# Optimization experiments

Measured on AMD Instinct MI355X. Metric: run time of the kernel, lower is better.

## Reference

```python
import jax, jax.numpy as jnp
import numpy as np

EPS = 1e-5

def gcn_conv(x, W, b, src, dst, ew, N):
    # PyG GCNConv: linear, add self-loops (weight 1), symmetric norm, aggregate, + bias
    xw = x @ W                                            # [N, C]
    deg = jax.ops.segment_sum(ew, dst, num_segments=N) + 1.0
    dis = jax.lax.rsqrt(deg)                              # deg^{-1/2}, deg >= 1
    coef = dis[src] * dis[dst] * ew                       # [E]
    msg = jax.ops.segment_sum(coef[:, None] * xw[src], dst, num_segments=N)
    return msg + (dis * dis)[:, None] * xw + b            # self-loop term + bias


def stride_pool(x, src, dst, ew, stride):
    # pad nodes to multiple of stride with zeros, mean over groups of `stride`,
    # keep only edges whose endpoints are both multiples of stride (weight mask)
    N, C = x.shape
    newN = -(-N // stride)
    pad = newN * stride - N
    if pad > 0:
        x = jnp.concatenate([x, jnp.zeros((pad, C), x.dtype)], axis=0)
    x = x.reshape(newN, stride, C).mean(axis=1)
    mask = (src % stride == 0) & (dst % stride == 0)
    src = jnp.minimum(src // stride, newN - 1)
    dst = jnp.minimum(dst // stride, newN - 1)
    ew = ew * mask.astype(ew.dtype)
    return x, src, dst, ew, newN


def bn_relu(x, g, b):
    # BatchNorm1d in training mode: batch stats over node dim, biased variance
    mu = x.mean(axis=0)
    var = x.var(axis=0)
    return jax.nn.relu((x - mu) * jax.lax.rsqrt(var + EPS) * g + b)


def setup_inputs() -> dict:
    key = jax.random.key(0)
    ks = jax.random.split(key, 16)
    N, E = 100000, 1600000
    inp = {
        'x': jax.random.normal(ks[0], (N, 1), jnp.float32),
        'W1': jax.random.normal(ks[1], (1, 64), jnp.float32) * 0.5,
        'b1': jax.random.normal(ks[2], (64,), jnp.float32) * 0.1,
        'g1': jnp.ones((64,), jnp.float32), 'be1': jnp.zeros((64,), jnp.float32),
        'W2': jax.random.normal(ks[3], (64, 64), jnp.float32) * 0.125,
        'b2': jax.random.normal(ks[4], (64,), jnp.float32) * 0.1,
        'g2': jnp.ones((64,), jnp.float32), 'be2': jnp.zeros((64,), jnp.float32),
        'W3': jax.random.normal(ks[5], (64, 64), jnp.float32) * 0.125,
        'b3': jax.random.normal(ks[6], (64,), jnp.float32) * 0.1,
        'g3': jnp.ones((64,), jnp.float32), 'be3': jnp.zeros((64,), jnp.float32),
        'W4': jax.random.normal(ks[7], (64, 64), jnp.float32) * 0.125,
        'b4': jax.random.normal(ks[8], (64,), jnp.float32) * 0.1,
        'g4': jnp.ones((64,), jnp.float32), 'be4': jnp.zeros((64,), jnp.float32),
        'fcW1': jax.random.normal(ks[9], (64, 128), jnp.float32) * 0.125,
        'fcb1': jax.random.normal(ks[10], (128,), jnp.float32) * 0.1,
        'fcW2': jax.random.normal(ks[11], (128, 10), jnp.float32) * 0.09,
        'fcb2': jax.random.normal(ks[12], (10,), jnp.float32) * 0.1,
        'src': jax.random.randint(ks[13], (E,), 0, N, jnp.int32).astype(jnp.int64),
        'dst': jax.random.randint(ks[14], (E,), 0, N, jnp.int32).astype(jnp.int64),
        'batch': jnp.zeros((N,), jnp.int64),
    }
    return inp


def reference(x, W1, b1, g1, be1, W2, b2, g2, be2, W3, b3, g3, be3,
              W4, b4, g4, be4, fcW1, fcb1, fcW2, fcb2, src, dst, batch):
    N0 = x.shape[0]
    ew = jnp.ones(src.shape, x.dtype)
    N = N0
    strides = [2, 2, 3, 3]
    params = [(W1, b1, g1, be1), (W2, b2, g2, be2), (W3, b3, g3, be3), (W4, b4, g4, be4)]
    for (W, b, g, be), s in zip(params, strides):
        x = gcn_conv(x, W, b, src, dst, ew, N)
        x, src, dst, ew, N = stride_pool(x, src, dst, ew, s)
        x = bn_relu(x, g, be)
    # pad back to original node count with zeros
    pad = N0 - x.shape[0]
    if pad > 0:
        x = jnp.concatenate([x, jnp.zeros((pad, x.shape[1]), x.dtype)], axis=0)
    # batch remapped to arange(N0) => global_mean_pool is identity
    x = jax.nn.relu(x @ fcW1 + fcb1)
    return x @ fcW2 + fcb2   # [N0, 10]
```

## Files before the change

kernel.cpp:

```cpp
#include <hip/hip_runtime.h>
#include <hip/hip_bf16.h>

#define GEPS 1e-5f

#define NN0 100000
#define NN1 50000
#define NN2 25000
#define NN3 8334
#define NN4 2778
#define BASE2 0
#define BASE3 50000
#define BASE4 75000
#define CNT_TOT 83334
#define CAPTOT 688128
#define NB 391
#define CAP_B 5120
#define BIN_CH 4096

__device__ __forceinline__ void atomAddF(float* p, float v) {
  unsafeAtomicAdd(p, v);
}

__device__ __forceinline__ unsigned ld_idx(const int* a, int e, int f64) {
  return (unsigned)(f64 ? a[2 * e] : a[e]);
}

__device__ __forceinline__ unsigned f2bf(float f) {
  unsigned b = __float_as_uint(f);
  return (b + 0x8000u) >> 16;
}

__global__ void gcn_init(int* cntAll, float* sumbuf, int* gcur, int* flag, const int* src) {
  int i = blockIdx.x * 256 + threadIdx.x;
  if (i == 0) {
    int o = src[1] | src[3] | src[5] | src[7] | src[9] | src[11] | src[13] | src[15];
    flag[0] = (o == 0) ? 1 : 0;
  }
  if (i < CNT_TOT) cntAll[i] = 0;
  if (i < 512) sumbuf[i] = 0.0f;
  if (i < NB) gcur[i] = i * CAP_B;
}

__global__ __launch_bounds__(256) void gcn_bin(const int* src, const int* dst, const int* flag,
                                               int* gcur, unsigned long long* bucketBuf, int E) {
  __shared__ unsigned long long els[BIN_CH];
  __shared__ int hist[NB];
  __shared__ int bcur[NB];
  int tid = threadIdx.x;
  for (int i = tid; i < NB; i += 256) hist[i] = 0;
  __syncthreads();
  int f = flag[0];
  int i0 = blockIdx.x * BIN_CH;
#pragma unroll
  for (int k = 0; k < BIN_CH / 256; ++k) {
    int e = i0 + k * 256 + tid;
    unsigned long long v = ~0ull;
    if (e < E) {
      unsigned s = ld_idx(src, e, f), d = ld_idx(dst, e, f);
      v = (unsigned long long)s | ((unsigned long long)d << 32);
      atomicAdd(&hist[d >> 8], 1);
    }
    els[k * 256 + tid] = v;
  }
  __syncthreads();
  for (int i = tid; i < NB; i += 256) {
    int c = hist[i];
    bcur[i] = (c > 0) ? atomicAdd(&gcur[i], c) : 0;
  }
  __syncthreads();
#pragma unroll
  for (int k = 0; k < BIN_CH / 256; ++k) {
    unsigned long long v = els[k * 256 + tid];
    if (v == ~0ull) continue;
    unsigned d = (unsigned)(v >> 32);
    int b = d >> 8;
    int pos = atomicAdd(&bcur[b], 1);
    if (pos < (b + 1) * CAP_B) bucketBuf[pos] = v;
  }
}

__global__ __launch_bounds__(256) void gcn_b1(const unsigned long long* bucketBuf, const int* gcur,
                                              float* deg1, int* cntAll) {
  int b = blockIdx.x, tid = threadIdx.x;
  int base_d = b << 8;
  __shared__ int ldeg[256];
  __shared__ int lc2[128];
  __shared__ int lc3[64];
  if (tid < 256) ldeg[tid] = 0;
  if (tid < 128) lc2[tid] = 0;
  if (tid < 64) lc3[tid] = 0;
  __syncthreads();
  int cnt = gcur[b] - b * CAP_B;
  if (cnt > CAP_B) cnt = CAP_B;
  const unsigned long long* eb = bucketBuf + (size_t)b * CAP_B;
  for (int e = tid; e < cnt; e += 256) {
    unsigned long long v = eb[e];
    unsigned s = (unsigned)v, d = (unsigned)(v >> 32);
    atomicAdd(&ldeg[d - base_d], 1);
    if (((s | d) & 1u) == 0u) atomicAdd(&lc2[(d >> 1) - (b << 7)], 1);
    if (((s | d) & 3u) == 0u) atomicAdd(&lc3[(d >> 2) - (b << 6)], 1);
    if ((s % 12u) == 0u && (d % 12u) == 0u) atomicAdd(&cntAll[BASE4 + d / 12u], 1);
  }
  __syncthreads();
  int nd = NN0 - base_d; if (nd > 256) nd = 256;
  if (tid < nd) deg1[base_d + tid] = (float)(ldeg[tid] + 1);
  int n2 = NN1 - (b << 7); if (n2 > 128) n2 = 128;
  if (tid < n2) cntAll[BASE2 + (b << 7) + tid] = lc2[tid];
  int n3 = NN2 - (b << 6); if (n3 > 64) n3 = 64;
  if (tid < n3) cntAll[BASE3 + (b << 6) + tid] = lc3[tid];
}

__global__ void gcn_scan_blocks(const int* __restrict__ cnt, int* __restrict__ out,
                                int* __restrict__ bsum, int n) {
  __shared__ int lds[256];
  int tid = threadIdx.x;
  int base = blockIdx.x * 1024 + tid * 4;
  int v0 = (base + 0 < n) ? cnt[base + 0] : 0;
  int v1 = (base + 1 < n) ? cnt[base + 1] : 0;
  int v2 = (base + 2 < n) ? cnt[base + 2] : 0;
  int v3 = (base + 3 < n) ? cnt[base + 3] : 0;
  int t = v0 + v1 + v2 + v3;
  lds[tid] = t;
  __syncthreads();
  for (int off = 1; off < 256; off <<= 1) {
    int add = (tid >= off) ? lds[tid - off] : 0;
    __syncthreads();
    lds[tid] += add;
    __syncthreads();
  }
  int excl = lds[tid] - t;
  if (base + 0 < n) out[base + 0] = excl;
  if (base + 1 < n) out[base + 1] = excl + v0;
  if (base + 2 < n) out[base + 2] = excl + v0 + v1;
  if (base + 3 < n) out[base + 3] = excl + v0 + v1 + v2;
  if (tid == 255) bsum[blockIdx.x] = lds[255];
}

__global__ void gcn_scan_tops(int* bsum, int nb, int* total_out) {
  __shared__ int lds[128];
  int tid = threadIdx.x;
  int v = (tid < nb) ? bsum[tid] : 0;
  lds[tid] = v;
  __syncthreads();
  for (int off = 1; off < 128; off <<= 1) {
    int add = (tid >= off) ? lds[tid - off] : 0;
    __syncthreads();
    lds[tid] += add;
    __syncthreads();
  }
  if (tid < nb) bsum[tid] = lds[tid] - v;
  if (tid == nb - 1) total_out[0] = lds[tid];
}

__global__ void gcn_scan_fix_u(int* off, int* cur, const int* bsum, const int* cnt,
                               float* disAll, const float* x, const float* deg1, float* u) {
  int i = blockIdx.x * 256 + threadIdx.x;
  if (i < CNT_TOT) {
    int v = off[i] + bsum[i >> 10];
    off[i] = v;
    cur[i] = v;
    disAll[i] = rsqrtf((float)(cnt[i] + 1));
  }
  if (i < NN0) u[i] = x[i] * rsqrtf(deg1[i]);
}

__global__ __launch_bounds__(256) void gcn_b2(const unsigned long long* bucketBuf, const int* gcur,
                                              const float* deg1, const float* u, const float* x,
                                              const int* offAll, int* curAll, unsigned* csrAll,
                                              float* tm, float* sumbuf) {
  int b = blockIdx.x, tid = threadIdx.x;
  int base_d = b << 8;
  __shared__ float acc[256];
  __shared__ float ldis[256];
  __shared__ int cur2[128];
  __shared__ int cur3[64];
  __shared__ float r1[256], r2[256];
  int nd = NN0 - base_d; if (nd > 256) nd = 256;
  int n2 = NN1 - (b << 7); if (n2 > 128) n2 = 128;
  int n3 = NN2 - (b << 6); if (n3 > 64) n3 = 64;
  acc[tid] = 0.0f;
  if (tid < nd) ldis[tid] = rsqrtf(deg1[base_d + tid]);
  if (tid < n2) cur2[tid] = offAll[BASE2 + (b << 7) + tid];
  if (tid < n3) cur3[tid] = offAll[BASE3 + (b << 6) + tid];
  __syncthreads();
  int cnt = gcur[b] - b * CAP_B;
  if (cnt > CAP_B) cnt = CAP_B;
  const unsigned long long* eb = bucketBuf + (size_t)b * CAP_B;
  for (int e = tid; e < cnt; e += 256) {
    unsigned long long v = eb[e];
    unsigned s = (unsigned)v, d = (unsigned)(v >> 32);
    atomicAdd(&acc[d - base_d], u[s]);
    if (((s | d) & 1u) == 0u) {
      int p = atomicAdd(&cur2[(d >> 1) - (b << 7)], 1);
      csrAll[p] = s >> 1;
    }
    if (((s | d) & 3u) == 0u) {
      int p = atomicAdd(&cur3[(d >> 2) - (b << 6)], 1);
      csrAll[p] = s >> 2;
    }
    if ((s % 12u) == 0u && (d % 12u) == 0u) {
      int p = atomicAdd(&curAll[BASE4 + d / 12u], 1);
      if (p < CAPTOT) csrAll[p] = s / 12u;
    }
  }
  __syncthreads();
  float tv = 0.0f;
  if (tid < n2) {
    int i0 = 2 * tid, i1 = 2 * tid + 1;
    float t0 = ldis[i0] * (acc[i0] + x[base_d + i0] * ldis[i0]);
    float t1 = ldis[i1] * (acc[i1] + x[base_d + i1] * ldis[i1]);
    tv = 0.5f * (t0 + t1);
    tm[(b << 7) + tid] = tv;
  }
  r1[tid] = tv; r2[tid] = tv * tv;
  __syncthreads();
  for (int o = 128; o > 0; o >>= 1) {
    if (tid < o) { r1[tid] += r1[tid + o]; r2[tid] += r2[tid + o]; }
    __syncthreads();
  }
  if (tid == 0) { atomAddF(&sumbuf[0], r1[0]); atomAddF(&sumbuf[1], r2[0]); }
}

__global__ void gcn_pack(unsigned* csr, const int* __restrict__ offAll,
                         const float* __restrict__ disAll) {
  int e = blockIdx.x * 256 + threadIdx.x;
  int tot = offAll[CNT_TOT];
  if (e >= tot) return;
  int b3 = offAll[BASE3], b4 = offAll[BASE4];
  int base = (e < b3) ? BASE2 : ((e < b4) ? BASE3 : BASE4);
  unsigned s = csr[e];
  float dis = disAll[base + (int)s];
  csr[e] = (s & 0xFFFFu) | (f2bf(dis) << 16);
}

__global__ __launch_bounds__(256) void gcn_zfill(const float* __restrict__ in, float* __restrict__ z,
                                                 const float* __restrict__ sumbuf, int sb,
                                                 const float* __restrict__ g_, const float* __restrict__ be,
                                                 const float* __restrict__ W1, int mode, int N, float invN) {
  int total = N * 64;
  for (int i = blockIdx.x * 256 + threadIdx.x; i < total; i += gridDim.x * 256) {
    int c = i & 63;
    float alpha, beta;
    if (mode == 0) {
      float mu = sumbuf[0] * invN;
      float var = sumbuf[1] * invN - mu * mu;
      float w = W1[c];
      alpha = w * rsqrtf(w * w * var + GEPS) * g_[c];
      beta = be[c] - mu * alpha;
      z[i] = fmaxf(fmaf(in[i >> 6], alpha, beta), 0.0f);
    } else {
      float mu = sumbuf[sb + c] * invN;
      float var = sumbuf[sb + 64 + c] * invN - mu * mu;
      alpha = rsqrtf(var + GEPS) * g_[c];
      beta = be[c] - mu * alpha;
      z[i] = fmaxf(fmaf(in[i], alpha, beta), 0.0f);
    }
  }
}

__global__ __launch_bounds__(256) void gcn_aggpool4(const float4* __restrict__ z, float4* __restrict__ q,
                                                    const float* __restrict__ disAll,
                                                    const int* __restrict__ offAll,
                                                    const unsigned* __restrict__ csr,
                                                    int base, int Nin, int Nout, int stride) {
  int tid = threadIdx.x;
  int lane = tid & 63, wid = tid >> 6;
  int g = (lane >> 4) & 3, li = lane & 15;
  float inv = 1.0f / (float)stride;
  for (int j = blockIdx.x * 4 + wid; j < Nout; j += gridDim.x * 4) {
    int r0 = j * stride;
    int rend = r0 + stride; if (rend > Nin) rend = Nin;
    float ax = 0.f, ay = 0.f, az = 0.f, aw = 0.f;
    if (r0 + g < rend) {
      float dr = disAll[base + r0 + g];
      float4 v = z[(size_t)(r0 + g) * 16 + li];
      float c = dr * dr;
      ax = fmaf(c, v.x, ax); ay = fmaf(c, v.y, ay);
      az = fmaf(c, v.z, az); aw = fmaf(c, v.w, aw);
    }
    for (int r = r0; r < rend; ++r) {
      float dr = disAll[base + r];
      int st = offAll[base + r], en = offAll[base + r + 1];
      for (int e0 = st; e0 < en; e0 += 8) {
        int ea = e0 + g, eb = e0 + 4 + g;
        unsigned pka = (ea < en) ? csr[ea] : 0u;
        unsigned pkb = (eb < en) ? csr[eb] : 0u;
        float4 va = z[(size_t)(pka & 0xFFFFu) * 16 + li];
        float4 vb = z[(size_t)(pkb & 0xFFFFu) * 16 + li];
        float ca = (ea < en) ? __uint_as_float(pka & 0xFFFF0000u) * dr : 0.0f;
        float cb = (eb < en) ? __uint_as_float(pkb & 0xFFFF0000u) * dr : 0.0f;
        ax = fmaf(ca, va.x, ax); ay = fmaf(ca, va.y, ay);
        az = fmaf(ca, va.z, az); aw = fmaf(ca, va.w, aw);
        ax = fmaf(cb, vb.x, ax); ay = fmaf(cb, vb.y, ay);
        az = fmaf(cb, vb.z, az); aw = fmaf(cb, vb.w, aw);
      }
    }
    ax += __shfl_xor(ax, 16); ay += __shfl_xor(ay, 16);
    az += __shfl_xor(az, 16); aw += __shfl_xor(aw, 16);
    ax += __shfl_xor(ax, 32); ay += __shfl_xor(ay, 32);
    az += __shfl_xor(az, 32); aw += __shfl_xor(aw, 32);
    if (g == 0) {
      float4 res;
      res.x = ax * inv; res.y = ay * inv; res.z = az * inv; res.w = aw * inv;
      q[(size_t)j * 16 + li] = res;
    }
  }
}

__global__ __launch_bounds__(256) void gcn_gemm_post(const float* __restrict__ q, const float* __restrict__ W,
                                                     const float* __restrict__ bias, float* __restrict__ p,
                                                     float* sumbuf, int sb, int Nin, int stride, int N) {
  __shared__ float Wl[4096];
  __shared__ float r1[256], r2[256];
  int tid = threadIdx.x;
  for (int i = tid; i < 4096; i += 256) Wl[i] = W[i];
  __syncthreads();
  int lane = tid & 63, wid = tid >> 6;
  float bl = bias[lane];
  float inv = 1.0f / (float)stride;
  float s = 0.f, ss = 0.f;
  for (int j = blockIdx.x * 4 + wid; j < N; j += gridDim.x * 4) {
    float zr = q[j * 64 + lane];
    int present = Nin - j * stride; if (present > stride) present = stride;
    float acc = bl * ((float)present * inv);
#pragma unroll
    for (int k = 0; k < 64; ++k) {
      float a = __shfl(zr, k);
      acc = fmaf(a, Wl[k * 64 + lane], acc);
    }
    p[j * 64 + lane] = acc;
    s += acc; ss += acc * acc;
  }
  r1[tid] = s; r2[tid] = ss;
  __syncthreads();
  if (tid < 64) {
    atomAddF(&sumbuf[sb + tid], r1[tid] + r1[tid + 64] + r1[tid + 128] + r1[tid + 192]);
    atomAddF(&sumbuf[sb + 64 + tid], r2[tid] + r2[tid + 64] + r2[tid + 128] + r2[tid + 192]);
  }
}

__global__ __launch_bounds__(256) void gcn_fc1(const float* __restrict__ z, const float* __restrict__ W,
                                               const float* __restrict__ bias, const float* __restrict__ fcW2,
                                               const float* __restrict__ fcb2, const float* __restrict__ sumbuf,
                                               const float* __restrict__ g_, const float* __restrict__ be,
                                               float* __restrict__ h, float* cpad, int N) {
  __shared__ float Wl[8192];
  int tid = threadIdx.x;
  for (int i = tid; i < 8192; i += 256) Wl[i] = W[i];
  if (blockIdx.x == 0 && tid < 10) {
    float acc = fcb2[tid];
    for (int k = 0; k < 128; ++k) acc = fmaf(fmaxf(bias[k], 0.0f), fcW2[k * 10 + tid], acc);
    cpad[tid] = acc;
  }
  int lane = tid & 63, wid = tid >> 6;
  float invN = 1.0f / (float)N;
  float mu = sumbuf[320 + lane] * invN;
  float var = sumbuf[320 + 64 + lane] * invN - mu * mu;
  float alpha = rsqrtf(var + GEPS) * g_[lane];
  float beta = be[lane] - mu * alpha;
  __syncthreads();
  for (int n = blockIdx.x * 4 + wid; n < N; n += gridDim.x * 4) {
    float zr = fmaxf(fmaf(z[n * 64 + lane], alpha, beta), 0.0f);
    float a0 = bias[lane], a1 = bias[64 + lane];
#pragma unroll
    for (int k = 0; k < 64; ++k) {
      float a = __shfl(zr, k);
      a0 = fmaf(a, Wl[k * 128 + lane], a0);
      a1 = fmaf(a, Wl[k * 128 + 64 + lane], a1);
    }
    h[n * 128 + lane] = fmaxf(a0, 0.0f);
    h[n * 128 + 64 + lane] = fmaxf(a1, 0.0f);
  }
}

__global__ __launch_bounds__(256) void gcn_fc2(const float* __restrict__ h, const float* __restrict__ W2,
                                               const float* __restrict__ b2, const float* __restrict__ cpad,
                                               float* __restrict__ out) {
  int idx = blockIdx.x * 256 + threadIdx.x;
  if (idx >= NN0 * 10) return;
  int n = idx / 10, o = idx - n * 10;
  if (n >= NN4) { out[idx] = cpad[o]; return; }
  float acc = b2[o];
  for (int k = 0; k < 128; ++k) acc = fmaf(h[n * 128 + k], W2[k * 10 + o], acc);
  out[idx] = acc;
}

extern "C" void kernel_launch(void* const* d_in, const int* in_sizes, int n_in,
                              void* d_out, int out_size, void* d_ws, size_t ws_size,
                              hipStream_t stream) {
  const float* x    = (const float*)d_in[0];
  const float* W1   = (const float*)d_in[1];
  const float* g1   = (const float*)d_in[3];
  const float* be1  = (const float*)d_in[4];
  const float* W2   = (const float*)d_in[5];
  const float* b2   = (const float*)d_in[6];
  const float* g2   = (const float*)d_in[7];
  const float* be2  = (const float*)d_in[8];
  const float* W3   = (const float*)d_in[9];
  const float* b3   = (const float*)d_in[10];
  const float* g3   = (const float*)d_in[11];
  const float* be3  = (const float*)d_in[12];
  const float* W4   = (const float*)d_in[13];
  const float* b4   = (const float*)d_in[14];
  const float* g4   = (const float*)d_in[15];
  const float* be4  = (const float*)d_in[16];
  const float* fcW1 = (const float*)d_in[17];
  const float* fcb1 = (const float*)d_in[18];
  const float* fcW2 = (const float*)d_in[19];
  const float* fcb2 = (const float*)d_in[20];
  const int*   src  = (const int*)d_in[21];
  const int*   dst  = (const int*)d_in[22];
  int E = in_sizes[21];
  float* out = (float*)d_out;

  char* w = (char*)d_ws;
  size_t off = 0;
  auto alloc = [&](size_t bytes) { size_t r = off; off = (off + bytes + 255) & ~(size_t)255; return (void*)(w + r); };
  float*    tm     = (float*)alloc(NN1 * 4);
  float*    deg1   = (float*)alloc(NN0 * 4);
  float*    u      = (float*)alloc(NN0 * 4);
  int*      cntAll = (int*)alloc((CNT_TOT + 8) * 4);
  int*      offAll = (int*)alloc((CNT_TOT + 8) * 4);
  int*      curAll = (int*)alloc((CNT_TOT + 8) * 4);
  float*    disAll = (float*)alloc((CNT_TOT + 8) * 4);
  int*      bsum   = (int*)alloc(128 * 4);
  float*    sumbuf = (float*)alloc(512 * 4);
  int*      flag   = (int*)alloc(256);
  int*      gcur   = (int*)alloc((NB + 8) * 4);
  unsigned* csrAll = (unsigned*)alloc((size_t)CAPTOT * 4);
  float*    h      = (float*)alloc((size_t)NN4 * 128 * 4);
  float*    q      = (float*)alloc((size_t)NN2 * 64 * 4);
  float*    p      = (float*)alloc((size_t)NN2 * 64 * 4);
  char*     big    = (char*)alloc((size_t)NB * CAP_B * 8);
  unsigned long long* bucketBuf = (unsigned long long*)big;
  float*    z      = (float*)big;
  float*    cpad   = sumbuf + 448;

  int bingrid = (E + BIN_CH - 1) / BIN_CH;
  int nscanb = (CNT_TOT + 1023) / 1024;

  hipLaunchKernelGGL(gcn_init, dim3(326), dim3(256), 0, stream, cntAll, sumbuf, gcur, flag, src);
  hipLaunchKernelGGL(gcn_bin, dim3(bingrid), dim3(256), 0, stream, src, dst, flag, gcur, bucketBuf, E);
  hipLaunchKernelGGL(gcn_b1, dim3(NB), dim3(256), 0, stream, bucketBuf, gcur, deg1, cntAll);
  hipLaunchKernelGGL(gcn_scan_blocks, dim3(nscanb), dim3(256), 0, stream, cntAll, offAll, bsum, CNT_TOT);
  hipLaunchKernelGGL(gcn_scan_tops, dim3(1), dim3(128), 0, stream, bsum, nscanb, offAll + CNT_TOT);
  hipLaunchKernelGGL(gcn_scan_fix_u, dim3(391), dim3(256), 0, stream,
                     offAll, curAll, bsum, cntAll, disAll, x, deg1, u);
  hipLaunchKernelGGL(gcn_b2, dim3(NB), dim3(256), 0, stream, bucketBuf, gcur, deg1, u, x,
                     offAll, curAll, csrAll, tm, sumbuf);
  hipLaunchKernelGGL(gcn_pack, dim3((CAPTOT + 255) / 256), dim3(256), 0, stream,
                     csrAll, offAll, disAll);

  hipLaunchKernelGGL(gcn_zfill, dim3(2048), dim3(256), 0, stream,
                     tm, z, sumbuf, 0, g1, be1, W1, 0, NN1, 1.0f / NN1);
  hipLaunchKernelGGL(gcn_aggpool4, dim3(2048), dim3(256), 0, stream,
                     (const float4*)z, (float4*)q, disAll, offAll, csrAll, BASE2, NN1, NN2, 2);
  hipLaunchKernelGGL(gcn_gemm_post, dim3(1024), dim3(256), 0, stream,
                     q, W2, b2, p, sumbuf, 64, NN1, 2, NN2);

  hipLaunchKernelGGL(gcn_zfill, dim3(2048), dim3(256), 0, stream,
                     p, z, sumbuf, 64, g2, be2, W1, 1, NN2, 1.0f / NN2);
  hipLaunchKernelGGL(gcn_aggpool4, dim3(1024), dim3(256), 0, stream,
                     (const float4*)z, (float4*)q, disAll, offAll, csrAll, BASE3, NN2, NN3, 3);
  hipLaunchKernelGGL(gcn_gemm_post, dim3(695), dim3(256), 0, stream,
                     q, W3, b3, p, sumbuf, 192, NN2, 3, NN3);

  hipLaunchKernelGGL(gcn_zfill, dim3(2048), dim3(256), 0, stream,
                     p, z, sumbuf, 192, g3, be3, W1, 1, NN3, 1.0f / NN3);
  hipLaunchKernelGGL(gcn_aggpool4, dim3(695), dim3(256), 0, stream,
                     (const float4*)z, (float4*)q, disAll, offAll, csrAll, BASE4, NN3, NN4, 3);
  hipLaunchKernelGGL(gcn_gemm_post, dim3(695), dim3(256), 0, stream,
                     q, W4, b4, p, sumbuf, 320, NN3, 3, NN4);

  hipLaunchKernelGGL(gcn_fc1, dim3(695), dim3(256), 0, stream,
                     p, fcW1, fcb1, fcW2, fcb2, sumbuf, g4, be4, h, cpad, NN4);
  hipLaunchKernelGGL(gcn_fc2, dim3((NN0 * 10 + 255) / 256), dim3(256), 0, stream,
                     h, fcW2, fcb2, cpad, out);
}
```

Before: 233.0 us.

## Fuse GCN pipeline stages: local-sorted binning, atomic CSR offsets, agg+gemm, fused FC

In the binning kernel, edges are now sorted by bucket in shared memory before the global write, so bucketBuf stores are coalesced. The three-kernel prefix scan is replaced by per-block scans that take CSR offsets through a global atomic counter, and the separate pack pass is removed by writing bf16-packed dis values while the CSR is built. Aggregation+pool is fused with the 64x64 GEMM, and both FC layers are fused, with a separate fill for the padded rows. This cuts the launch count and intermediate buffer traffic. The trade-off is that CSR segment order now depends on atomic ordering, and the fused kernels use more registers and LDS.

```diff
diff --git a/kernel.cpp b/kernel.cpp
--- a/kernel.cpp
+++ b/kernel.cpp
@@ -35,6 +35,7 @@
   if (i == 0) {
     int o = src[1] | src[3] | src[5] | src[7] | src[9] | src[11] | src[13] | src[15];
     flag[0] = (o == 0) ? 1 : 0;
+    flag[1] = 0;
   }
   if (i < CNT_TOT) cntAll[i] = 0;
   if (i < 512) sumbuf[i] = 0.0f;
@@ -43,16 +44,21 @@
 
 __global__ __launch_bounds__(256) void gcn_bin(const int* src, const int* dst, const int* flag,
                                                int* gcur, unsigned long long* bucketBuf, int E) {
-  __shared__ unsigned long long els[BIN_CH];
+  __shared__ unsigned long long sorted[BIN_CH];
   __shared__ int hist[NB];
+  __shared__ int scanb[NB];
+  __shared__ int gbase[NB];
   __shared__ int bcur[NB];
+  __shared__ int h2[256];
   int tid = threadIdx.x;
   for (int i = tid; i < NB; i += 256) hist[i] = 0;
   __syncthreads();
   int f = flag[0];
   int i0 = blockIdx.x * BIN_CH;
+  int nvalid = E - i0; if (nvalid > BIN_CH) nvalid = BIN_CH; if (nvalid < 0) nvalid = 0;
+  unsigned long long ev[16];
 #pragma unroll
-  for (int k = 0; k < BIN_CH / 256; ++k) {
+  for (int k = 0; k < 16; ++k) {
     int e = i0 + k * 256 + tid;
     unsigned long long v = ~0ull;
     if (e < E) {
@@ -60,38 +66,62 @@
       v = (unsigned long long)s | ((unsigned long long)d << 32);
       atomicAdd(&hist[d >> 8], 1);
     }
-    els[k * 256 + tid] = v;
-  }
+    ev[k] = v;
+  }
+  __syncthreads();
+  int a0 = (2 * tid < NB) ? hist[2 * tid] : 0;
+  int a1 = (2 * tid + 1 < NB) ? hist[2 * tid + 1] : 0;
+  int t = a0 + a1;
+  h2[tid] = t;
+  __syncthreads();
+  for (int o = 1; o < 256; o <<= 1) {
+    int add = (tid >= o) ? h2[tid - o] : 0;
+    __syncthreads();
+    h2[tid] += add;
+    __syncthreads();
+  }
+  int ex = h2[tid] - t;
+  if (2 * tid < NB) scanb[2 * tid] = ex;
+  if (2 * tid + 1 < NB) scanb[2 * tid + 1] = ex + a0;
   __syncthreads();
   for (int i = tid; i < NB; i += 256) {
     int c = hist[i];
-    bcur[i] = (c > 0) ? atomicAdd(&gcur[i], c) : 0;
+    gbase[i] = c ? atomicAdd(&gcur[i], c) : 0;
+    bcur[i] = scanb[i];
   }
   __syncthreads();
 #pragma unroll
-  for (int k = 0; k < BIN_CH / 256; ++k) {
-    unsigned long long v = els[k * 256 + tid];
+  for (int k = 0; k < 16; ++k) {
+    unsigned long long v = ev[k];
     if (v == ~0ull) continue;
-    unsigned d = (unsigned)(v >> 32);
-    int b = d >> 8;
+    int b = (int)((unsigned)(v >> 32) >> 8);
     int pos = atomicAdd(&bcur[b], 1);
-    if (pos < (b + 1) * CAP_B) bucketBuf[pos] = v;
+    sorted[pos] = v;
+  }
+  __syncthreads();
+  for (int i = tid; i < nvalid; i += 256) {
+    unsigned long long v = sorted[i];
+    int b = (int)((unsigned)(v >> 32) >> 8);
+    size_t ad = (size_t)gbase[b] + (i - scanb[b]);
+    if (ad < (size_t)(b + 1) * CAP_B) bucketBuf[ad] = v;
   }
 }
 
 __global__ __launch_bounds__(256) void gcn_b1(const unsigned long long* bucketBuf, const int* gcur,
-                                              float* deg1, int* cntAll) {
+                                              float* deg1, int* cntAll, int* offAll, float* disAll,
+                                              int* gCsr) {
   int b = blockIdx.x, tid = threadIdx.x;
   int base_d = b << 8;
   __shared__ int ldeg[256];
   __shared__ int lc2[128];
   __shared__ int lc3[64];
-  if (tid < 256) ldeg[tid] = 0;
+  __shared__ int scn[256];
+  __shared__ int sbase;
+  ldeg[tid] = 0;
   if (tid < 128) lc2[tid] = 0;
   if (tid < 64) lc3[tid] = 0;
   __syncthreads();
-  int cnt = gcur[b] - b * CAP_B;
-  if (cnt > CAP_B) cnt = CAP_B;
+  int cnt = gcur[b] - b * CAP_B; if (cnt > CAP_B) cnt = CAP_B;
   const unsigned long long* eb = bucketBuf + (size_t)b * CAP_B;
   for (int e = tid; e < cnt; e += 256) {
     unsigned long long v = eb[e];
@@ -102,72 +132,64 @@
     if ((s % 12u) == 0u && (d % 12u) == 0u) atomicAdd(&cntAll[BASE4 + d / 12u], 1);
   }
   __syncthreads();
+  int c = (tid < 128) ? lc2[tid] : ((tid < 192) ? lc3[tid - 128] : 0);
+  scn[tid] = c;
+  __syncthreads();
+  for (int o = 1; o < 256; o <<= 1) {
+    int add = (tid >= o) ? scn[tid - o] : 0;
+    __syncthreads();
+    scn[tid] += add;
+    __syncthreads();
+  }
+  if (tid == 255) sbase = (scn[255] > 0) ? atomicAdd(gCsr, scn[255]) : 0;
+  __syncthreads();
+  int start = sbase + scn[tid] - c;
   int nd = NN0 - base_d; if (nd > 256) nd = 256;
   if (tid < nd) deg1[base_d + tid] = (float)(ldeg[tid] + 1);
   int n2 = NN1 - (b << 7); if (n2 > 128) n2 = 128;
-  if (tid < n2) cntAll[BASE2 + (b << 7) + tid] = lc2[tid];
   int n3 = NN2 - (b << 6); if (n3 > 64) n3 = 64;
-  if (tid < n3) cntAll[BASE3 + (b << 6) + tid] = lc3[tid];
-}
-
-__global__ void gcn_scan_blocks(const int* __restrict__ cnt, int* __restrict__ out,
-                                int* __restrict__ bsum, int n) {
-  __shared__ int lds[256];
-  int tid = threadIdx.x;
-  int base = blockIdx.x * 1024 + tid * 4;
-  int v0 = (base + 0 < n) ? cnt[base + 0] : 0;
-  int v1 = (base + 1 < n) ? cnt[base + 1] : 0;
-  int v2 = (base + 2 < n) ? cnt[base + 2] : 0;
-  int v3 = (base + 3 < n) ? cnt[base + 3] : 0;
-  int t = v0 + v1 + v2 + v3;
-  lds[tid] = t;
-  __syncthreads();
-  for (int off = 1; off < 256; off <<= 1) {
-    int add = (tid >= off) ? lds[tid - off] : 0;
-    __syncthreads();
-    lds[tid] += add;
-    __syncthreads();
-  }
-  int excl = lds[tid] - t;
-  if (base + 0 < n) out[base + 0] = excl;
-  if (base + 1 < n) out[base + 1] = excl + v0;
-  if (base + 2 < n) out[base + 2] = excl + v0 + v1;
-  if (base + 3 < n) out[base + 3] = excl + v0 + v1 + v2;
-  if (tid == 255) bsum[blockIdx.x] = lds[255];
-}
-
-__global__ void gcn_scan_tops(int* bsum, int nb, int* total_out) {
-  __shared__ int lds[128];
-  int tid = threadIdx.x;
-  int v = (tid < nb) ? bsum[tid] : 0;
-  lds[tid] = v;
-  __syncthreads();
-  for (int off = 1; off < 128; off <<= 1) {
-    int add = (tid >= off) ? lds[tid - off] : 0;
-    __syncthreads();
-    lds[tid] += add;
-    __syncthreads();
-  }
-  if (tid < nb) bsum[tid] = lds[tid] - v;
-  if (tid == nb - 1) total_out[0] = lds[tid];
-}
-
-__global__ void gcn_scan_fix_u(int* off, int* cur, const int* bsum, const int* cnt,
-                               float* disAll, const float* x, const float* deg1, float* u) {
-  int i = blockIdx.x * 256 + threadIdx.x;
-  if (i < CNT_TOT) {
-    int v = off[i] + bsum[i >> 10];
-    off[i] = v;
-    cur[i] = v;
-    disAll[i] = rsqrtf((float)(cnt[i] + 1));
-  }
+  if (tid < n2) {
+    int idx = BASE2 + (b << 7) + tid;
+    offAll[idx] = start; cntAll[idx] = c; disAll[idx] = rsqrtf((float)(c + 1));
+  }
+  if (tid >= 128 && tid < 128 + n3) {
+    int idx = BASE3 + (b << 6) + (tid - 128);
+    offAll[idx] = start; cntAll[idx] = c; disAll[idx] = rsqrtf((float)(c + 1));
+  }
+}
+
+__global__ void gcn_ufill(const float* x, const float* deg1, float* u,
+                          const int* cntAll, int* offAll, float* disAll, int* cur4, int* gCsr) {
+  int b = blockIdx.x, tid = threadIdx.x;
+  int i = b * 256 + tid;
   if (i < NN0) u[i] = x[i] * rsqrtf(deg1[i]);
+  if (b < (NN3 + 255) / 256) {
+    __shared__ int scn[256];
+    __shared__ int sbase;
+    int c = (i < NN3) ? cntAll[BASE4 + i] : 0;
+    scn[tid] = c;
+    __syncthreads();
+    for (int o = 1; o < 256; o <<= 1) {
+      int add = (tid >= o) ? scn[tid - o] : 0;
+      __syncthreads();
+      scn[tid] += add;
+      __syncthreads();
+    }
+    if (tid == 255) sbase = (scn[255] > 0) ? atomicAdd(gCsr, scn[255]) : 0;
+    __syncthreads();
+    if (i < NN3) {
+      int start = sbase + scn[tid] - c;
+      offAll[BASE4 + i] = start;
+      cur4[i] = start;
+      disAll[BASE4 + i] = rsqrtf((float)(c + 1));
+    }
+  }
 }
 
 __global__ __launch_bounds__(256) void gcn_b2(const unsigned long long* bucketBuf, const int* gcur,
                                               const float* deg1, const float* u, const float* x,
-                                              const int* offAll, int* curAll, unsigned* csrAll,
-                                              float* tm, float* sumbuf) {
+                                              const int* offAll, const float* disAll, int* cur4,
+                                              unsigned* csrAll, float* tm, float* sumbuf) {
   int b = blockIdx.x, tid = threadIdx.x;
   int base_d = b << 8;
   __shared__ float acc[256];
@@ -183,24 +205,26 @@
   if (tid < n2) cur2[tid] = offAll[BASE2 + (b << 7) + tid];
   if (tid < n3) cur3[tid] = offAll[BASE3 + (b << 6) + tid];
   __syncthreads();
-  int cnt = gcur[b] - b * CAP_B;
-  if (cnt > CAP_B) cnt = CAP_B;
+  int cnt = gcur[b] - b * CAP_B; if (cnt > CAP_B) cnt = CAP_B;
   const unsigned long long* eb = bucketBuf + (size_t)b * CAP_B;
   for (int e = tid; e < cnt; e += 256) {
     unsigned long long v = eb[e];
     unsigned s = (unsigned)v, d = (unsigned)(v >> 32);
     atomicAdd(&acc[d - base_d], u[s]);
     if (((s | d) & 1u) == 0u) {
+      unsigned sp = s >> 1;
       int p = atomicAdd(&cur2[(d >> 1) - (b << 7)], 1);
-      csrAll[p] = s >> 1;
+      if ((unsigned)p < CAPTOT) csrAll[p] = sp | (f2bf(disAll[BASE2 + sp]) << 16);
     }
     if (((s | d) & 3u) == 0u) {
+      unsigned sp = s >> 2;
       int p = atomicAdd(&cur3[(d >> 2) - (b << 6)], 1);
-      csrAll[p] = s >> 2;
+      if ((unsigned)p < CAPTOT) csrAll[p] = sp | (f2bf(disAll[BASE3 + sp]) << 16);
     }
     if ((s % 12u) == 0u && (d % 12u) == 0u) {
-      int p = atomicAdd(&curAll[BASE4 + d / 12u], 1);
-      if (p < CAPTOT) csrAll[p] = s / 12u;
+      unsigned sp = s / 12u;
+      int p = atomicAdd(&cur4[d / 12u], 1);
+      if ((unsigned)p < CAPTOT) csrAll[p] = sp | (f2bf(disAll[BASE4 + sp]) << 16);
     }
   }
   __syncthreads();
@@ -219,18 +243,6 @@
     __syncthreads();
   }
   if (tid == 0) { atomAddF(&sumbuf[0], r1[0]); atomAddF(&sumbuf[1], r2[0]); }
-}
-
-__global__ void gcn_pack(unsigned* csr, const int* __restrict__ offAll,
-                         const float* __restrict__ disAll) {
-  int e = blockIdx.x * 256 + threadIdx.x;
-  int tot = offAll[CNT_TOT];
-  if (e >= tot) return;
-  int b3 = offAll[BASE3], b4 = offAll[BASE4];
-  int base = (e < b3) ? BASE2 : ((e < b4) ? BASE3 : BASE4);
-  unsigned s = csr[e];
-  float dis = disAll[base + (int)s];
-  csr[e] = (s & 0xFFFFu) | (f2bf(dis) << 16);
 }
 
 __global__ __launch_bounds__(256) void gcn_zfill(const float* __restrict__ in, float* __restrict__ z,
@@ -258,15 +270,25 @@
   }
 }
 
-__global__ __launch_bounds__(256) void gcn_aggpool4(const float4* __restrict__ z, float4* __restrict__ q,
+__global__ __launch_bounds__(256) void gcn_agg_gemm(const float4* __restrict__ z, float* __restrict__ p,
                                                     const float* __restrict__ disAll,
                                                     const int* __restrict__ offAll,
+                                                    const int* __restrict__ cntAll,
                                                     const unsigned* __restrict__ csr,
-                                                    int base, int Nin, int Nout, int stride) {
+                                                    const float* __restrict__ W,
+                                                    const float* __restrict__ bias,
+                                                    int base, int Nin, int Nout, int stride,
+                                                    float* sumbuf, int sb) {
+  __shared__ float Wl[4096];
+  __shared__ float r1[256], r2[256];
   int tid = threadIdx.x;
+  for (int i = tid; i < 4096; i += 256) Wl[i] = W[i];
   int lane = tid & 63, wid = tid >> 6;
-  int g = (lane >> 4) & 3, li = lane & 15;
+  int g = lane >> 4, li = lane & 15;
   float inv = 1.0f / (float)stride;
+  float bl = bias[lane];
+  float s = 0.f, ss = 0.f;
+  __syncthreads();
   for (int j = blockIdx.x * 4 + wid; j < Nout; j += gridDim.x * 4) {
     int r0 = j * stride;
     int rend = r0 + stride; if (rend > Nin) rend = Nin;
@@ -275,12 +297,11 @@
       float dr = disAll[base + r0 + g];
       float4 v = z[(size_t)(r0 + g) * 16 + li];
       float c = dr * dr;
-      ax = fmaf(c, v.x, ax); ay = fmaf(c, v.y, ay);
-      az = fmaf(c, v.z, az); aw = fmaf(c, v.w, aw);
+      ax = c * v.x; ay = c * v.y; az = c * v.z; aw = c * v.w;
     }
     for (int r = r0; r < rend; ++r) {
       float dr = disAll[base + r];
-      int st = offAll[base + r], en = offAll[base + r + 1];
+      int st = offAll[base + r], en = st + cntAll[base + r];
       for (int e0 = st; e0 < en; e0 += 8) {
         int ea = e0 + g, eb = e0 + 4 + g;
         unsigned pka = (ea < en) ? csr[ea] : 0u;
@@ -299,36 +320,19 @@
     az += __shfl_xor(az, 16); aw += __shfl_xor(aw, 16);
     ax += __shfl_xor(ax, 32); ay += __shfl_xor(ay, 32);
     az += __shfl_xor(az, 32); aw += __shfl_xor(aw, 32);
-    if (g == 0) {
-      float4 res;
-      res.x = ax * inv; res.y = ay * inv; res.z = az * inv; res.w = aw * inv;
-      q[(size_t)j * 16 + li] = res;
-    }
-  }
-}
-
-__global__ __launch_bounds__(256) void gcn_gemm_post(const float* __restrict__ q, const float* __restrict__ W,
-                                                     const float* __restrict__ bias, float* __restrict__ p,
-                                                     float* sumbuf, int sb, int Nin, int stride, int N) {
-  __shared__ float Wl[4096];
-  __shared__ float r1[256], r2[256];
-  int tid = threadIdx.x;
-  for (int i = tid; i < 4096; i += 256) Wl[i] = W[i];
-  __syncthreads();
-  int lane = tid & 63, wid = tid >> 6;
-  float bl = bias[lane];
-  float inv = 1.0f / (float)stride;
-  float s = 0.f, ss = 0.f;
-  for (int j = blockIdx.x * 4 + wid; j < N; j += gridDim.x * 4) {
-    float zr = q[j * 64 + lane];
-    int present = Nin - j * stride; if (present > stride) present = stride;
+    ax *= inv; ay *= inv; az *= inv; aw *= inv;
+    int present = rend - r0;
     float acc = bl * ((float)present * inv);
 #pragma unroll
-    for (int k = 0; k < 64; ++k) {
-      float a = __shfl(zr, k);
-      acc = fmaf(a, Wl[k * 64 + lane], acc);
-    }
-    p[j * 64 + lane] = acc;
+    for (int l = 0; l < 16; ++l) {
+      float bx = __shfl(ax, l), by = __shfl(ay, l);
+      float bz = __shfl(az, l), bw = __shfl(aw, l);
+      acc = fmaf(bx, Wl[(4 * l + 0) * 64 + lane], acc);
+      acc = fmaf(by, Wl[(4 * l + 1) * 64 + lane], acc);
+      acc = fmaf(bz, Wl[(4 * l + 2) * 64 + lane], acc);
+      acc = fmaf(bw, Wl[(4 * l + 3) * 64 + lane], acc);
+    }
+    p[(size_t)j * 64 + lane] = acc;
     s += acc; ss += acc * acc;
   }
   r1[tid] = s; r2[tid] = ss;
@@ -339,50 +343,78 @@
   }
 }
 
-__global__ __launch_bounds__(256) void gcn_fc1(const float* __restrict__ z, const float* __restrict__ W,
-                                               const float* __restrict__ bias, const float* __restrict__ fcW2,
-                                               const float* __restrict__ fcb2, const float* __restrict__ sumbuf,
-                                               const float* __restrict__ g_, const float* __restrict__ be,
-                                               float* __restrict__ h, float* cpad, int N) {
+__global__ __launch_bounds__(256) void gcn_fc(const float* __restrict__ pin, const float* __restrict__ W1f,
+                                              const float* __restrict__ b1f, const float* __restrict__ W2f,
+                                              const float* __restrict__ b2f, const float* __restrict__ sumbuf,
+                                              const float* __restrict__ g_, const float* __restrict__ be,
+                                              float* __restrict__ outp) {
   __shared__ float Wl[8192];
+  __shared__ float W2l[1280];
   int tid = threadIdx.x;
-  for (int i = tid; i < 8192; i += 256) Wl[i] = W[i];
-  if (blockIdx.x == 0 && tid < 10) {
-    float acc = fcb2[tid];
-    for (int k = 0; k < 128; ++k) acc = fmaf(fmaxf(bias[k], 0.0f), fcW2[k * 10 + tid], acc);
-    cpad[tid] = acc;
-  }
+  for (int i = tid; i < 8192; i += 256) Wl[i] = W1f[i];
+  for (int i = tid; i < 1280; i += 256) W2l[i] = W2f[i];
   int lane = tid & 63, wid = tid >> 6;
-  float invN = 1.0f / (float)N;
+  float invN = 1.0f / (float)NN4;
   float mu = sumbuf[320 + lane] * invN;
   float var = sumbuf[320 + 64 + lane] * invN - mu * mu;
   float alpha = rsqrtf(var + GEPS) * g_[lane];
   float beta = be[lane] - mu * alpha;
   __syncthreads();
-  for (int n = blockIdx.x * 4 + wid; n < N; n += gridDim.x * 4) {
-    float zr = fmaxf(fmaf(z[n * 64 + lane], alpha, beta), 0.0f);
-    float a0 = bias[lane], a1 = bias[64 + lane];
+  for (int n = blockIdx.x * 4 + wid; n < NN4; n += gridDim.x * 4) {
+    float zr = fmaxf(fmaf(pin[n * 64 + lane], alpha, beta), 0.0f);
+    float a0 = b1f[lane], a1 = b1f[64 + lane];
 #pragma unroll
     for (int k = 0; k < 64; ++k) {
       float a = __shfl(zr, k);
       a0 = fmaf(a, Wl[k * 128 + lane], a0);
       a1 = fmaf(a, Wl[k * 128 + 64 + lane], a1);
     }
-    h[n * 128 + lane] = fmaxf(a0, 0.0f);
-    h[n * 128 + 64 + lane] = fmaxf(a1, 0.0f);
-  }
-}
-
-__global__ __launch_bounds__(256) void gcn_fc2(const float* __restrict__ h, const float* __restrict__ W2,
-                                               const float* __restrict__ b2, const float* __restrict__ cpad,
-                                               float* __restrict__ out) {
-  int idx = blockIdx.x * 256 + threadIdx.x;
-  if (idx >= NN0 * 10) return;
-  int n = idx / 10, o = idx - n * 10;
-  if (n >= NN4) { out[idx] = cpad[o]; return; }
-  float acc = b2[o];
-  for (int k = 0; k < 128; ++k) acc = fmaf(h[n * 128 + k], W2[k * 10 + o], acc);
-  out[idx] = acc;
+    a0 = fmaxf(a0, 0.f); a1 = fmaxf(a1, 0.f);
+    float o0, o1, o2, o3, o4, o5, o6, o7, o8, o9;
+    o0 = fmaf(a0, W2l[lane * 10 + 0], a1 * W2l[(64 + lane) * 10 + 0]);
+    o1 = fmaf(a0, W2l[lane * 10 + 1], a1 * W2l[(64 + lane) * 10 + 1]);
+    o2 = fmaf(a0, W2l[lane * 10 + 2], a1 * W2l[(64 + lane) * 10 + 2]);
+    o3 = fmaf(a0, W2l[lane * 10 + 3], a1 * W2l[(64 + lane) * 10 + 3]);
+    o4 = fmaf(a0, W2l[lane * 10 + 4], a1 * W2l[(64 + lane) * 10 + 4]);
+    o5 = fmaf(a0, W2l[lane * 10 + 5], a1 * W2l[(64 + lane) * 10 + 5]);
+    o6 = fmaf(a0, W2l[lane * 10 + 6], a1 * W2l[(64 + lane) * 10 + 6]);
+    o7 = fmaf(a0, W2l[lane * 10 + 7], a1 * W2l[(64 + lane) * 10 + 7]);
+    o8 = fmaf(a0, W2l[lane * 10 + 8], a1 * W2l[(64 + lane) * 10 + 8]);
+    o9 = fmaf(a0, W2l[lane * 10 + 9], a1 * W2l[(64 + lane) * 10 + 9]);
+#pragma unroll
+    for (int m = 1; m < 64; m <<= 1) {
+      o0 += __shfl_xor(o0, m); o1 += __shfl_xor(o1, m); o2 += __shfl_xor(o2, m);
+      o3 += __shfl_xor(o3, m); o4 += __shfl_xor(o4, m); o5 += __shfl_xor(o5, m);
+      o6 += __shfl_xor(o6, m); o7 += __shfl_xor(o7, m); o8 += __shfl_xor(o8, m);
+      o9 += __shfl_xor(o9, m);
+    }
+    if (lane < 10) {
+      float v = o9;
+      switch (lane) {
+        case 0: v = o0; break; case 1: v = o1; break; case 2: v = o2; break;
+        case 3: v = o3; break; case 4: v = o4; break; case 5: v = o5; break;
+        case 6: v = o6; break; case 7: v = o7; break; case 8: v = o8; break;
+        default: break;
+      }
+      outp[n * 10 + lane] = v + b2f[lane];
+    }
+  }
+}
+
+__global__ __launch_bounds__(256) void gcn_fill(const float* __restrict__ b1f, const float* __restrict__ W2f,
+                                                const float* __restrict__ b2f, float* __restrict__ outp) {
+  __shared__ float cv[10];
+  int tid = threadIdx.x;
+  if (tid < 10) {
+    float acc = b2f[tid];
+    for (int k = 0; k < 128; ++k) acc = fmaf(fmaxf(b1f[k], 0.0f), W2f[k * 10 + tid], acc);
+    cv[tid] = acc;
+  }
+  __syncthreads();
+  int total = (NN0 - NN4) * 10;
+  for (int i = blockIdx.x * 256 + tid; i < total; i += gridDim.x * 256) {
+    outp[NN4 * 10 + i] = cv[i % 10];
+  }
 }
 
 extern "C" void kernel_launch(void* const* d_in, const int* in_sizes, int n_in,
@@ -421,59 +453,47 @@
   float*    u      = (float*)alloc(NN0 * 4);
   int*      cntAll = (int*)alloc((CNT_TOT + 8) * 4);
   int*      offAll = (int*)alloc((CNT_TOT + 8) * 4);
-  int*      curAll = (int*)alloc((CNT_TOT + 8) * 4);
   float*    disAll = (float*)alloc((CNT_TOT + 8) * 4);
-  int*      bsum   = (int*)alloc(128 * 4);
+  int*      cur4   = (int*)alloc((NN3 + 8) * 4);
   float*    sumbuf = (float*)alloc(512 * 4);
   int*      flag   = (int*)alloc(256);
   int*      gcur   = (int*)alloc((NB + 8) * 4);
   unsigned* csrAll = (unsigned*)alloc((size_t)CAPTOT * 4);
-  float*    h      = (float*)alloc((size_t)NN4 * 128 * 4);
-  float*    q      = (float*)alloc((size_t)NN2 * 64 * 4);
   float*    p      = (float*)alloc((size_t)NN2 * 64 * 4);
   char*     big    = (char*)alloc((size_t)NB * CAP_B * 8);
   unsigned long long* bucketBuf = (unsigned long long*)big;
   float*    z      = (float*)big;
-  float*    cpad   = sumbuf + 448;
+  int*      gCsr   = flag + 1;
 
   int bingrid = (E + BIN_CH - 1) / BIN_CH;
-  int nscanb = (CNT_TOT + 1023) / 1024;
 
   hipLaunchKernelGGL(gcn_init, dim3(326), dim3(256), 0, stream, cntAll, sumbuf, gcur, flag, src);
   hipLaunchKernelGGL(gcn_bin, dim3(bingrid), dim3(256), 0, stream, src, dst, flag, gcur, bucketBuf, E);
-  hipLaunchKernelGGL(gcn_b1, dim3(NB), dim3(256), 0, stream, bucketBuf, gcur, deg1, cntAll);
-  hipLaunchKernelGGL(gcn_scan_blocks, dim3(nscanb), dim3(256), 0, stream, cntAll, offAll, bsum, CNT_TOT);
-  hipLaunchKernelGGL(gcn_scan_tops, dim3(1), dim3(128), 0, stream, bsum, nscanb, offAll + CNT_TOT);
-  hipLaunchKernelGGL(gcn_scan_fix_u, dim3(391), dim3(256), 0, stream,
-                     offAll, curAll, bsum, cntAll, disAll, x, deg1, u);
-  hipLaunchKernelGGL(gcn_b2, dim3(NB), dim3(256), 0, stream, bucketBuf, gcur, deg1, u, x,
-                     offAll, curAll, csrAll, tm, sumbuf);
-  hipLaunchKernelGGL(gcn_pack, dim3((CAPTOT + 255) / 256), dim3(256), 0, stream,
-                     csrAll, offAll, disAll);
+  hipLaunchKernelGGL(gcn_b1, dim3(NB), dim3(256), 0, stream,
+                     bucketBuf, gcur, deg1, cntAll, offAll, disAll, gCsr);
+  hipLaunchKernelGGL(gcn_ufill, dim3(391), dim3(256), 0, stream,
+                     x, deg1, u, cntAll, offAll, disAll, cur4, gCsr);
+  hipLaunchKernelGGL(gcn_b2, dim3(NB), dim3(256), 0, stream,
+                     bucketBuf, gcur, deg1, u, x, offAll, disAll, cur4, csrAll, tm, sumbuf);
 
   hipLaunchKernelGGL(gcn_zfill, dim3(2048), dim3(256), 0, stream,
                      tm, z, sumbuf, 0, g1, be1, W1, 0, NN1, 1.0f / NN1);
-  hipLaunchKernelGGL(gcn_aggpool4, dim3(2048), dim3(256), 0, stream,
-                     (const float4*)z, (float4*)q, disAll, offAll, csrAll, BASE2, NN1, NN2, 2);
-  hipLaunchKernelGGL(gcn_gemm_post, dim3(1024), dim3(256), 0, stream,
-                     q, W2, b2, p, sumbuf, 64, NN1, 2, NN2);
-
+  hipLaunchKernelGGL(gcn_agg_gemm, dim3(2048), dim3(256), 0, stream,
+                     (const float4*)z, p, disAll, offAll, cntAll, csrAll, W2, b2,
+                     BASE2, NN1, NN2, 2, sumbuf, 64);
   hipLaunchKernelGGL(gcn_zfill, dim3(2048), dim3(256), 0, stream,
                      p, z, sumbuf, 64, g2, be2, W1, 1, NN2, 1.0f / NN2);
-  hipLaunchKernelGGL(gcn_aggpool4, dim3(1024), dim3(256), 0, stream,
-                     (const float4*)z, (float4*)q, disAll, offAll, csrAll, BASE3, NN2, NN3, 3);
-  hipLaunchKernelGGL(gcn_gemm_post, dim3(695), dim3(256), 0, stream,
-                     q, W3, b3, p, sumbuf, 192, NN2, 3, NN3);
-
+  hipLaunchKernelGGL(gcn_agg_gemm, dim3(2048), dim3(256), 0, stream,
+                     (const float4*)z, p, disAll, offAll, cntAll, csrAll, W3, b3,
+                     BASE3, NN2, NN3, 3, sumbuf, 192);
   hipLaunchKernelGGL(gcn_zfill, dim3(2048), dim3(256), 0, stream,
                      p, z, sumbuf, 192, g3, be3, W1, 1, NN3, 1.0f / NN3);
-  hipLaunchKernelGGL(gcn_aggpool4, dim3(695), dim3(256), 0, stream,
-                     (const float4*)z, (float4*)q, disAll, offAll, csrAll, BASE4, NN3, NN4, 3);
-  hipLaunchKernelGGL(gcn_gemm_post, dim3(695), dim3(256), 0, stream,
-                     q, W4, b4, p, sumbuf, 320, NN3, 3, NN4);
-
-  hipLaunchKernelGGL(gcn_fc1, dim3(695), dim3(256), 0, stream,
-                     p, fcW1, fcb1, fcW2, fcb2, sumbuf, g4, be4, h, cpad, NN4);
-  hipLaunchKernelGGL(gcn_fc2, dim3((NN0 * 10 + 255) / 256), dim3(256), 0, stream,
-                     h, fcW2, fcb2, cpad, out);
-}
+  hipLaunchKernelGGL(gcn_agg_gemm, dim3(695), dim3(256), 0, stream,
+                     (const float4*)z, p, disAll, offAll, cntAll, csrAll, W4, b4,
+                     BASE4, NN3, NN4, 3, sumbuf, 320);
+
+  hipLaunchKernelGGL(gcn_fc, dim3(695), dim3(256), 0, stream,
+                     p, fcW1, fcb1, fcW2, fcb2, sumbuf, g4, be4, out);
+  hipLaunchKernelGGL(gcn_fill, dim3(2048), dim3(256), 0, stream,
+                     fcb1, fcW2, fcb2, out);
+}
```

Measured after the change: 267.1 us. 1.15x slower.
